# Kernel optimization log

Measured on AMD Instinct MI355X. Metric: run time of the kernel, lower is better.

## Reference

```python
import jax, jax.numpy as jnp
import numpy as np

N_NODES = 20000
N_EDGES = 50000
NF = 64
NG = 5
N_CONV = 2


def setup_inputs() -> dict:
    key = jax.random.key(0)
    ks = jax.random.split(key, 20)
    s = 0.1
    return {
        "h": jax.random.normal(ks[0], (N_NODES, 64), jnp.float32),
        "edge_index": jax.random.randint(ks[1], (2, N_EDGES), 0, N_NODES, jnp.int64),
        "edge_weight": jax.random.uniform(ks[2], (N_EDGES,), jnp.float32),
        "edge_attr": jax.random.normal(ks[3], (N_EDGES, NG), jnp.float32),
        # lin0: Linear(64 -> nf); stored as [in, out]
        "lin0_w": jax.random.normal(ks[4], (64, NF), jnp.float32) * s,
        "lin0_b": jnp.zeros((NF,), jnp.float32),
        # short: Linear(num_gaussians -> nf)
        "short_w": jax.random.normal(ks[5], (NG, NF), jnp.float32) * s,
        "short_b": jnp.zeros((NF,), jnp.float32),
        # edge network nn: Linear(nf -> nf//4) -> ReLU -> Linear(nf//4 -> nf*nf)
        "nn1_w": jax.random.normal(ks[6], (NF, NF // 4), jnp.float32) * s,
        "nn1_b": jnp.zeros((NF // 4,), jnp.float32),
        "nn2_w": jax.random.normal(ks[7], (NF // 4, NF * NF), jnp.float32) * s,
        "nn2_b": jnp.zeros((NF * NF,), jnp.float32),
        # NNConv root weight (Linear(nf, nf, bias=False)) + conv bias
        "root_w": jax.random.normal(ks[8], (NF, NF), jnp.float32) * s,
        "conv_bias": jnp.zeros((NF,), jnp.float32),
        # GRU(nf, nf): torch packs gates as [r; z; n] along dim 0 of [3*nf, nf]
        "gru_w_ih": jax.random.normal(ks[9], (NF, 3 * NF), jnp.float32) * s,
        "gru_w_hh": jax.random.normal(ks[10], (NF, 3 * NF), jnp.float32) * s,
        "gru_b_ih": jnp.zeros((3 * NF,), jnp.float32),
        "gru_b_hh": jnp.zeros((3 * NF,), jnp.float32),
    }


def _gru_cell(x, h, w_ih, w_hh, b_ih, b_hh):
    gi = x @ w_ih + b_ih            # [N, 3*nf]
    gh = h @ w_hh + b_hh
    r = jax.nn.sigmoid(gi[:, :NF] + gh[:, :NF])
    z = jax.nn.sigmoid(gi[:, NF:2 * NF] + gh[:, NF:2 * NF])
    n = jnp.tanh(gi[:, 2 * NF:] + r * gh[:, 2 * NF:])
    return (1.0 - z) * n + z * h


def reference(h, edge_index, edge_weight, edge_attr,
              lin0_w, lin0_b, short_w, short_b,
              nn1_w, nn1_b, nn2_w, nn2_b,
              root_w, conv_bias,
              gru_w_ih, gru_w_hh, gru_b_ih, gru_b_hh):
    n_nodes = h.shape[0]
    src, dst = edge_index[0], edge_index[1]

    out = jax.nn.relu(h @ lin0_w + lin0_b)                       # [N, nf]
    ea = jax.nn.relu(edge_attr @ short_w + short_b)              # [E, nf]

    # edge-conditioned weights (fixed per forward since edge_attr is fixed)
    w_e = (jax.nn.relu(ea @ nn1_w + nn1_b) @ nn2_w + nn2_b)      # [E, nf*nf]
    w_e = w_e.reshape(-1, NF, NF)                                # [E, nf, nf]

    # scatter-mean denominator (clamped to 1 like PyG)
    cnt = jax.ops.segment_sum(jnp.ones_like(dst, jnp.float32), dst,
                              num_segments=n_nodes)
    cnt = jnp.maximum(cnt, 1.0)[:, None]                          # [N, 1]

    hidden = out                                                  # GRU state [N, nf]
    for _ in range(N_CONV):
        x_j = out[src]                                            # gather [E, nf]
        msg = jnp.einsum('ef,efg->eg', x_j, w_e)                  # per-edge matmul
        agg = jax.ops.segment_sum(msg, dst, num_segments=n_nodes) / cnt
        conv = agg + out @ root_w + conv_bias                     # root + bias
        m = jax.nn.relu(conv)
        hidden = _gru_cell(m, hidden, gru_w_ih, gru_w_hh, gru_b_ih, gru_b_hh)
        out = hidden
    return out
```

## Files before the change

kernel.cpp:

```cpp
#include <hip/hip_runtime.h>

#define N_NODES 20000
#define N_EDGES 50000
#define NPB 32
#define KCAP 16
#define NTILE (N_NODES / NPB)

#define ZB 79
#define PB 416
#define LB 625
#define ETB 1563
#define VB0 (ZB + PB + LB + ETB)
#define HB 196

typedef __attribute__((ext_vector_type(8))) short short8;
typedef __attribute__((ext_vector_type(4))) float f32x4;
typedef unsigned int u32;
typedef unsigned short u16;

#define SswzB(i, o) (((i) * 2304 + (o)) ^ (((i) & 7) << 4))
#define MofsB(i, o) ((36864 + (i) * 256 + (o)) ^ (((i) & 7) << 4))

struct Pars {
    const float* h; const int* ei; const float* eattr;
    const float *lin0w, *lin0b, *shw, *shb, *w1, *b1, *w2, *b2;
    const float *rootw, *convb, *wih, *whh, *bih, *bhh;
    u16 *X0b, *X1b;
    float* out;
    u16 *t_arr, *Bp1, *Bp2;
    int* cur; u32* edata;
};

__device__ inline u16 f2bf(float x) {
    u32 u = __float_as_uint(x);
    return (u16)((u + 0x7FFFu + ((u >> 16) & 1u)) >> 16);
}
__device__ inline float bf2f(u16 v) { return __uint_as_float((u32)v << 16); }

__device__ inline void acc_edge(float* acc, const u16* t, float x) {
    uint4 a = *(const uint4*)t, b = *(const uint4*)(t + 8);
    u32 tw[8] = {a.x, a.y, a.z, a.w, b.x, b.y, b.z, b.w};
#pragma unroll
    for (int q = 0; q < 8; ++q) {
        acc[2 * q]     += __uint_as_float(tw[q] << 16) * x;
        acc[2 * q + 1] += __uint_as_float(tw[q] & 0xFFFF0000u) * x;
    }
}

__global__ __launch_bounds__(256) void k_stageA(Pars p) {
    __shared__ float sh[32][64];
    int tid = threadIdx.x;
    int vb = blockIdx.x;
    if (vb < ZB) {
        int n = vb * 256 + tid;
        if (n < N_NODES) p.cur[n] = 0;
        return;
    }
    vb -= ZB;
    if (vb < PB) {
        int idx = vb * 256 + tid;
        if (idx < 73728) {
            int j = idx & 7, l = (idx >> 3) & 63, rest = idx >> 9;
            int kb = rest % 36, nt = rest / 36;
            int row = kb * 32 + (l >> 4) * 8 + j;
            int col = nt * 16 + (l & 15);
            float v;
            if (row < 1024) v = p.w2[row * 64 + col];
            else if (row < 1088) v = p.b2[(row - 1024) * 64 + col];
            else v = p.rootw[(row - 1088) * 64 + col];
            p.Bp1[idx] = f2bf(v);
        } else {
            int o = idx - 73728;
            int j = o & 7, l = (o >> 3) & 63, rest = o >> 9;
            int kb = rest & 3, nt = rest >> 2;
            int k2 = kb * 32 + (l >> 4) * 8 + j;
            int c = nt * 16 + (l & 15);
            float v;
            if (k2 < 64) {
                v = (c < 192) ? p.wih[k2 * 192 + c] : 0.f;
            } else {
                int f = k2 - 64;
                v = (c < 128) ? p.whh[f * 192 + c] : ((c < 192) ? 0.f : p.whh[f * 192 + c - 64]);
            }
            p.Bp2[o] = f2bf(v);
        }
        return;
    }
    vb -= PB;
    int g = tid & 63, q = tid >> 6;
    if (vb < LB) {
        int n0 = vb * 32;
        for (int i = tid; i < 32 * 64; i += 256) sh[i >> 6][i & 63] = p.h[n0 * 64 + i];
        __syncthreads();
        float bias = p.lin0b[g];
        float acc[8];
#pragma unroll
        for (int j = 0; j < 8; j++) acc[j] = bias;
        for (int f = 0; f < 64; f++) {
            float wv = p.lin0w[f * 64 + g];
#pragma unroll
            for (int j = 0; j < 8; j++) acc[j] += sh[q * 8 + j][f] * wv;
        }
#pragma unroll
        for (int j = 0; j < 8; j++) {
            float a = acc[j];
            p.X0b[(n0 + q * 8 + j) * 64 + g] = f2bf(a > 0.f ? a : 0.f);
        }
        return;
    }
    vb -= LB;
    {
        int e0 = vb * 32;
#pragma unroll
        for (int j = 0; j < 8; j++) {
            int r = q * 8 + j;
            int e = e0 + r;
            if (e < N_EDGES) {
                float a0 = p.eattr[e * 5 + 0], a1 = p.eattr[e * 5 + 1], a2 = p.eattr[e * 5 + 2],
                      a3 = p.eattr[e * 5 + 3], a4 = p.eattr[e * 5 + 4];
                float v = p.shb[g] + a0 * p.shw[g] + a1 * p.shw[64 + g] + a2 * p.shw[128 + g]
                        + a3 * p.shw[192 + g] + a4 * p.shw[256 + g];
                sh[r][g] = v > 0.f ? v : 0.f;
            }
        }
        __syncthreads();
#pragma unroll
        for (int jj = 0; jj < 2; jj++) {
            int r = q * 8 + (g >> 4) * 2 + jj;
            int e = e0 + r;
            int o = g & 15;
            if (e < N_EDGES) {
                float acc = p.b1[o];
                for (int c = 0; c < 64; c++) acc += sh[r][c] * p.w1[c * 16 + o];
                float t = acc > 0.f ? acc : 0.f;
                p.t_arr[(size_t)e * 16 + o] = f2bf(t);
            }
        }
    }
}

__global__ __launch_bounds__(256) void k_stageB(Pars p) {
    int e = blockIdx.x * 256 + threadIdx.x;
    if (e < N_EDGES) {
        int dn = p.ei[N_EDGES + e];
        int q = atomicAdd(&p.cur[dn], 1);
        if (q < KCAP) p.edata[dn * KCAP + q] = ((u32)e << 15) | (u32)p.ei[e];
    }
}

__global__ __launch_bounds__(512, 4) void k_convK(Pars p, const u16* __restrict__ Xprev,
                                                  u16* __restrict__ XoutB,
                                                  float* __restrict__ XoutF) {
    __shared__ __align__(16) char smem[73728];
    char* Sb = smem;
    float* G = (float*)smem;
    int tid = threadIdx.x, g = tid & 63, wq = tid >> 6;
    int m16 = g & 15, hi4 = g >> 4;
    int n0 = blockIdx.x * NPB;

    int cvv[4];
    u16 xrb[4];
    float ic4[4];
#pragma unroll
    for (int jj = 0; jj < 4; ++jj) {
        int n = n0 + wq * 4 + jj;
        int c = __builtin_amdgcn_readfirstlane(p.cur[n]);
        cvv[jj] = c < KCAP ? c : KCAP;
        ic4[jj] = 1.0f / (c > 0 ? (float)c : 1.0f);
        xrb[jj] = Xprev[n * 64 + g];
    }

#pragma unroll
    for (int jj = 0; jj < 4; ++jj) {
        int i = wq * 4 + jj;
        float acc[16];
#pragma unroll
        for (int k = 0; k < 16; ++k) acc[k] = 0.f;
        float sx = 0.f;
        int base = (n0 + i) * KCAP;
        int cv = cvv[jj];
        for (int pp = 0; pp < cv; pp += 4) {
            int m = cv - pp;
            uint4 ed = *(const uint4*)(p.edata + base + pp);
            u32 k0 = ed.x;
            u32 k1 = m > 1 ? ed.y : ed.x;
            u32 k2 = m > 2 ? ed.z : ed.x;
            u32 k3 = m > 3 ? ed.w : ed.x;
            float x0 = bf2f(Xprev[(k0 & 0x7FFFu) * 64 + g]);
            float x1 = m > 1 ? bf2f(Xprev[(k1 & 0x7FFFu) * 64 + g]) : 0.f;
            float x2 = m > 2 ? bf2f(Xprev[(k2 & 0x7FFFu) * 64 + g]) : 0.f;
            float x3 = m > 3 ? bf2f(Xprev[(k3 & 0x7FFFu) * 64 + g]) : 0.f;
            acc_edge(acc, p.t_arr + (size_t)(k0 >> 15) * 16, x0);
            acc_edge(acc, p.t_arr + (size_t)(k1 >> 15) * 16, x1);
            acc_edge(acc, p.t_arr + (size_t)(k2 >> 15) * 16, x2);
            acc_edge(acc, p.t_arr + (size_t)(k3 >> 15) * 16, x3);
            sx += x0 + x1 + x2 + x3;
        }
        float ic = ic4[jj];
#pragma unroll
        for (int k = 0; k < 16; ++k)
            *(u16*)(Sb + SswzB(i, k * 128 + g * 2)) = f2bf(acc[k] * ic);
        *(u16*)(Sb + SswzB(i, 2048 + g * 2)) = f2bf(sx * ic);
        *(u16*)(Sb + SswzB(i, 2176 + g * 2)) = xrb[jj];
    }
    __syncthreads();

    f32x4 d0 = {0.f, 0.f, 0.f, 0.f}, d1 = {0.f, 0.f, 0.f, 0.f};
    if (wq < 4) {
#pragma unroll
        for (int kb = 0; kb < 36; ++kb) {
            short8 b = *(const short8*)((const char*)p.Bp1 + ((size_t)(wq * 36 + kb) * 64 + g) * 16);
            short8 a0 = *(const short8*)(Sb + SswzB(m16, kb * 64 + hi4 * 16));
            short8 a1 = *(const short8*)(Sb + SswzB(16 + m16, kb * 64 + hi4 * 16));
            d0 = __builtin_amdgcn_mfma_f32_16x16x32_bf16(a0, b, d0, 0, 0, 0);
            d1 = __builtin_amdgcn_mfma_f32_16x16x32_bf16(a1, b, d1, 0, 0, 0);
        }
    }
    __syncthreads();

    if (wq < 4) {
        float cb = p.convb[wq * 16 + m16];
#pragma unroll
        for (int r = 0; r < 4; ++r) {
            float m0 = d0[r] + cb;
            m0 = m0 > 0.f ? m0 : 0.f;
            *(u16*)(smem + MofsB(hi4 * 4 + r, (wq * 16 + m16) * 2)) = f2bf(m0);
            float m1 = d1[r] + cb;
            m1 = m1 > 0.f ? m1 : 0.f;
            *(u16*)(smem + MofsB(16 + hi4 * 4 + r, (wq * 16 + m16) * 2)) = f2bf(m1);
        }
    }
    __syncthreads();

    if (wq < 4) {
        short8 a2[2][4];
#pragma unroll
        for (int mt = 0; mt < 2; ++mt) {
#pragma unroll
            for (int t = 0; t < 2; ++t)
                a2[mt][t] = *(const short8*)(smem + MofsB(mt * 16 + m16, t * 64 + hi4 * 16));
#pragma unroll
            for (int t = 0; t < 2; ++t)
                a2[mt][2 + t] = *(const short8*)(Xprev + (size_t)(n0 + mt * 16 + m16) * 64 + t * 32 + hi4 * 8);
        }
        f32x4 e4[2][4];
#pragma unroll
        for (int mt = 0; mt < 2; ++mt)
#pragma unroll
            for (int q = 0; q < 4; ++q) { e4[mt][q].x = 0.f; e4[mt][q].y = 0.f; e4[mt][q].z = 0.f; e4[mt][q].w = 0.f; }
#pragma unroll
        for (int q = 0; q < 4; ++q)
#pragma unroll
            for (int kb = 0; kb < 4; ++kb) {
                short8 b = *(const short8*)((const char*)p.Bp2 + ((size_t)((wq * 4 + q) * 4 + kb) * 64 + g) * 16);
                e4[0][q] = __builtin_amdgcn_mfma_f32_16x16x32_bf16(a2[0][kb], b, e4[0][q], 0, 0, 0);
                e4[1][q] = __builtin_amdgcn_mfma_f32_16x16x32_bf16(a2[1][kb], b, e4[1][q], 0, 0, 0);
            }
#pragma unroll
        for (int mt = 0; mt < 2; ++mt)
#pragma unroll
            for (int q = 0; q < 4; ++q)
#pragma unroll
                for (int r = 0; r < 4; ++r)
                    G[mt * 4160 + (hi4 * 4 + r) * 260 + wq * 64 + q * 16 + m16] = e4[mt][q][r];
    }
    __syncthreads();

    float b_r = p.bih[g] + p.bhh[g];
    float b_z = p.bih[64 + g] + p.bhh[64 + g];
    float b_gi = p.bih[128 + g];
    float b_gh = p.bhh[128 + g];
#pragma unroll
    for (int jj = 0; jj < 4; ++jj) {
        int i = wq * 4 + jj;
        int n = n0 + i;
        const float* Gi = G + (i >> 4) * 4160 + (i & 15) * 260;
        float rs = Gi[g] + b_r;
        float zs = Gi[64 + g] + b_z;
        float gi = Gi[128 + g] + b_gi;
        float gh = Gi[192 + g] + b_gh;
        float r = 1.f / (1.f + __expf(-rs));
        float z = 1.f / (1.f + __expf(-zs));
        float aa = gi + r * gh;
        float ex = __expf(2.f * aa);
        float nt = 1.f - 2.f / (ex + 1.f);
        float res = (1.f - z) * nt + z * bf2f(xrb[jj]);
        if (XoutF) XoutF[n * 64 + g] = res;
        else       XoutB[n * 64 + g] = f2bf(res);
    }
}

extern "C" void kernel_launch(void* const* d_in, const int* in_sizes, int n_in,
                              void* d_out, int out_size, void* d_ws, size_t ws_size,
                              hipStream_t stream) {
    Pars p;
    p.h     = (const float*)d_in[0];
    p.ei    = (const int*)d_in[1];
    p.eattr = (const float*)d_in[3];
    p.lin0w = (const float*)d_in[4];
    p.lin0b = (const float*)d_in[5];
    p.shw   = (const float*)d_in[6];
    p.shb   = (const float*)d_in[7];
    p.w1    = (const float*)d_in[8];
    p.b1    = (const float*)d_in[9];
    p.w2    = (const float*)d_in[10];
    p.b2    = (const float*)d_in[11];
    p.rootw = (const float*)d_in[12];
    p.convb = (const float*)d_in[13];
    p.wih   = (const float*)d_in[14];
    p.whh   = (const float*)d_in[15];
    p.bih   = (const float*)d_in[16];
    p.bhh   = (const float*)d_in[17];

    char* ws = (char*)d_ws;
    p.X0b   = (u16*)ws;   ws += (size_t)N_NODES * 64 * 2;
    p.X1b   = (u16*)ws;   ws += (size_t)N_NODES * 64 * 2;
    p.t_arr = (u16*)ws;   ws += (size_t)N_EDGES * 16 * 2;
    p.Bp1   = (u16*)ws;   ws += (size_t)73728 * 2;
    p.Bp2   = (u16*)ws;   ws += (size_t)32768 * 2;
    p.cur   = (int*)ws;   ws += (size_t)N_NODES * 4;
    p.edata = (u32*)ws;   ws += (size_t)N_NODES * KCAP * 4;
    p.out   = (float*)d_out;

    k_stageA<<<VB0, 256, 0, stream>>>(p);
    k_stageB<<<HB, 256, 0, stream>>>(p);
    k_convK<<<NTILE, 512, 0, stream>>>(p, p.X0b, p.X1b, nullptr);
    k_convK<<<NTILE, 512, 0, stream>>>(p, p.X1b, nullptr, p.out);
}
```

Before: 91.43 us.

## Split both conv-kernel GEMMs across all eight waves with LDS split-K reduction

```diff
diff --git a/kernel.cpp b/kernel.cpp
--- a/kernel.cpp
+++ b/kernel.cpp
@@ -19,7 +19,7 @@
 typedef unsigned short u16;
 
 #define SswzB(i, o) (((i) * 2304 + (o)) ^ (((i) & 7) << 4))
-#define MofsB(i, o) ((36864 + (i) * 256 + (o)) ^ (((i) & 7) << 4))
+#define MofsB(i, o) ((65536 + (i) * 256 + (o)) ^ (((i) & 7) << 4))
 
 struct Pars {
     const float* h; const int* ei; const float* eattr;
@@ -153,8 +153,10 @@
                                                   float* __restrict__ XoutF) {
     __shared__ __align__(16) char smem[73728];
     char* Sb = smem;
+    float* DP = (float*)smem;
     float* G = (float*)smem;
     int tid = threadIdx.x, g = tid & 63, wq = tid >> 6;
+    int nt = wq & 3, kh = wq >> 2;
     int m16 = g & 15, hi4 = g >> 4;
     int n0 = blockIdx.x * NPB;
 
@@ -206,42 +208,47 @@
     __syncthreads();
 
     f32x4 d0 = {0.f, 0.f, 0.f, 0.f}, d1 = {0.f, 0.f, 0.f, 0.f};
-    if (wq < 4) {
-#pragma unroll
-        for (int kb = 0; kb < 36; ++kb) {
-            short8 b = *(const short8*)((const char*)p.Bp1 + ((size_t)(wq * 36 + kb) * 64 + g) * 16);
-            short8 a0 = *(const short8*)(Sb + SswzB(m16, kb * 64 + hi4 * 16));
-            short8 a1 = *(const short8*)(Sb + SswzB(16 + m16, kb * 64 + hi4 * 16));
-            d0 = __builtin_amdgcn_mfma_f32_16x16x32_bf16(a0, b, d0, 0, 0, 0);
-            d1 = __builtin_amdgcn_mfma_f32_16x16x32_bf16(a1, b, d1, 0, 0, 0);
-        }
-    }
-    __syncthreads();
-
-    if (wq < 4) {
-        float cb = p.convb[wq * 16 + m16];
-#pragma unroll
-        for (int r = 0; r < 4; ++r) {
-            float m0 = d0[r] + cb;
-            m0 = m0 > 0.f ? m0 : 0.f;
-            *(u16*)(smem + MofsB(hi4 * 4 + r, (wq * 16 + m16) * 2)) = f2bf(m0);
-            float m1 = d1[r] + cb;
-            m1 = m1 > 0.f ? m1 : 0.f;
-            *(u16*)(smem + MofsB(16 + hi4 * 4 + r, (wq * 16 + m16) * 2)) = f2bf(m1);
-        }
-    }
-    __syncthreads();
-
-    if (wq < 4) {
-        short8 a2[2][4];
+#pragma unroll
+    for (int kk = 0; kk < 18; ++kk) {
+        int kb = kh * 18 + kk;
+        short8 b = *(const short8*)((const char*)p.Bp1 + ((size_t)(nt * 36 + kb) * 64 + g) * 16);
+        short8 a0 = *(const short8*)(Sb + SswzB(m16, kb * 64 + hi4 * 16));
+        short8 a1 = *(const short8*)(Sb + SswzB(16 + m16, kb * 64 + hi4 * 16));
+        d0 = __builtin_amdgcn_mfma_f32_16x16x32_bf16(a0, b, d0, 0, 0, 0);
+        d1 = __builtin_amdgcn_mfma_f32_16x16x32_bf16(a1, b, d1, 0, 0, 0);
+    }
+    __syncthreads();
+#pragma unroll
+    for (int r = 0; r < 4; ++r) {
+        DP[kh * 2048 + (hi4 * 4 + r) * 64 + nt * 16 + m16] = d0[r];
+        DP[kh * 2048 + 1024 + (hi4 * 4 + r) * 64 + nt * 16 + m16] = d1[r];
+    }
+    __syncthreads();
+
+#pragma unroll
+    for (int t2 = 0; t2 < 4; ++t2) {
+        int idx = tid + t2 * 512;
+        int i = idx >> 6, c = idx & 63;
+        int a = (i >> 4) * 1024 + (i & 15) * 64 + c;
+        float m = DP[a] + DP[2048 + a] + p.convb[c];
+        m = m > 0.f ? m : 0.f;
+        *(u16*)(smem + MofsB(i, c * 2)) = f2bf(m);
+    }
+    __syncthreads();
+
+    {
+        short8 a2[2][2];
 #pragma unroll
         for (int mt = 0; mt < 2; ++mt) {
-#pragma unroll
-            for (int t = 0; t < 2; ++t)
-                a2[mt][t] = *(const short8*)(smem + MofsB(mt * 16 + m16, t * 64 + hi4 * 16));
-#pragma unroll
-            for (int t = 0; t < 2; ++t)
-                a2[mt][2 + t] = *(const short8*)(Xprev + (size_t)(n0 + mt * 16 + m16) * 64 + t * 32 + hi4 * 8);
+            if (kh == 0) {
+#pragma unroll
+                for (int t = 0; t < 2; ++t)
+                    a2[mt][t] = *(const short8*)(smem + MofsB(mt * 16 + m16, t * 64 + hi4 * 16));
+            } else {
+#pragma unroll
+                for (int t = 0; t < 2; ++t)
+                    a2[mt][t] = *(const short8*)(Xprev + (size_t)(n0 + mt * 16 + m16) * 64 + t * 32 + hi4 * 8);
+            }
         }
         f32x4 e4[2][4];
 #pragma unroll
@@ -251,10 +258,11 @@
 #pragma unroll
         for (int q = 0; q < 4; ++q)
 #pragma unroll
-            for (int kb = 0; kb < 4; ++kb) {
-                short8 b = *(const short8*)((const char*)p.Bp2 + ((size_t)((wq * 4 + q) * 4 + kb) * 64 + g) * 16);
-                e4[0][q] = __builtin_amdgcn_mfma_f32_16x16x32_bf16(a2[0][kb], b, e4[0][q], 0, 0, 0);
-                e4[1][q] = __builtin_amdgcn_mfma_f32_16x16x32_bf16(a2[1][kb], b, e4[1][q], 0, 0, 0);
+            for (int t = 0; t < 2; ++t) {
+                int kb2 = kh * 2 + t;
+                short8 b = *(const short8*)((const char*)p.Bp2 + ((size_t)((nt * 4 + q) * 4 + kb2) * 64 + g) * 16);
+                e4[0][q] = __builtin_amdgcn_mfma_f32_16x16x32_bf16(a2[0][t], b, e4[0][q], 0, 0, 0);
+                e4[1][q] = __builtin_amdgcn_mfma_f32_16x16x32_bf16(a2[1][t], b, e4[1][q], 0, 0, 0);
             }
 #pragma unroll
         for (int mt = 0; mt < 2; ++mt)
@@ -262,7 +270,7 @@
             for (int q = 0; q < 4; ++q)
 #pragma unroll
                 for (int r = 0; r < 4; ++r)
-                    G[mt * 4160 + (hi4 * 4 + r) * 260 + wq * 64 + q * 16 + m16] = e4[mt][q][r];
+                    G[kh * 8192 + mt * 4096 + (hi4 * 4 + r) * 256 + nt * 64 + q * 16 + m16] = e4[mt][q][r];
     }
     __syncthreads();
 
@@ -274,17 +282,17 @@
     for (int jj = 0; jj < 4; ++jj) {
         int i = wq * 4 + jj;
         int n = n0 + i;
-        const float* Gi = G + (i >> 4) * 4160 + (i & 15) * 260;
-        float rs = Gi[g] + b_r;
-        float zs = Gi[64 + g] + b_z;
-        float gi = Gi[128 + g] + b_gi;
-        float gh = Gi[192 + g] + b_gh;
+        int base = (i >> 4) * 4096 + (i & 15) * 256;
+        float rs = G[base + g]        + G[8192 + base + g]        + b_r;
+        float zs = G[base + 64 + g]   + G[8192 + base + 64 + g]   + b_z;
+        float gi = G[base + 128 + g]  + G[8192 + base + 128 + g]  + b_gi;
+        float gh = G[base + 192 + g]  + G[8192 + base + 192 + g]  + b_gh;
         float r = 1.f / (1.f + __expf(-rs));
         float z = 1.f / (1.f + __expf(-zs));
         float aa = gi + r * gh;
         float ex = __expf(2.f * aa);
-        float nt = 1.f - 2.f / (ex + 1.f);
-        float res = (1.f - z) * nt + z * bf2f(xrb[jj]);
+        float nt2 = 1.f - 2.f / (ex + 1.f);
+        float res = (1.f - z) * nt2 + z * bf2f(xrb[jj]);
         if (XoutF) XoutF[n * 64 + g] = res;
         else       XoutB[n * 64 + g] = f2bf(res);
     }
```

New measurement: 90.57 us. No clear change (-0.9%).
